# Optimization experiments

Measured on AMD Instinct MI355X. Metric: run time of the kernel, lower is better.

Reference implementation:

```python
import jax, jax.numpy as jnp
import numpy as np

B, D, N = 2, 512, 2048
H, MQ, MV = 8, 64, 64
SCALE = 1.0 / np.sqrt(D).astype(np.float32)  # 1/sqrt(num_dim_q), full dim


def setup_inputs() -> dict:
    key = jax.random.key(0)
    ks = jax.random.split(key, 9)
    s = 0.02
    return {
        "Q": jax.random.normal(ks[0], (B, D, N), jnp.float32),
        "Wq": jax.random.normal(ks[1], (MQ * H, D), jnp.float32) * s,
        "bq": jnp.zeros((MQ * H,), jnp.float32),
        "Wk": jax.random.normal(ks[2], (MQ * H, D), jnp.float32) * s,
        "bk": jnp.zeros((MQ * H,), jnp.float32),
        "Wv": jax.random.normal(ks[3], (MV * H, D), jnp.float32) * s,
        "bv": jnp.zeros((MV * H,), jnp.float32),
        "Wo": jax.random.normal(ks[4], (D, MV * H), jnp.float32) * s,
        "bo": jnp.zeros((D,), jnp.float32),
    }


def _conv1x1(x, W, b):
    # Conv1d with kernel_size=1 == per-position linear: [B,Cin,N] -> [B,Cout,N]
    return jnp.einsum("bcn,oc->bon", x, W) + b[None, :, None]


def reference(Q, Wq, bq, Wk, bk, Wv, bv, Wo, bo):
    q = _conv1x1(Q, Wq, bq)  # [B, MQ*H, N]
    k = _conv1x1(Q, Wk, bk)
    v = _conv1x1(Q, Wv, bv)  # [B, MV*H, N]
    b = Q.shape[0]
    n = Q.shape[2]
    # channel index factors as (dim, head): channel = d*H + h (matches torch .view)
    q = q.reshape(b, MQ, H, n)
    k = k.reshape(b, MQ, H, n)
    v = v.reshape(b, MV, H, n)
    scores = jnp.einsum("bdhq,bdhk->bhqk", q, k) * SCALE  # [B,H,Nq,Nk]
    attn = jax.nn.softmax(scores, axis=-1)
    o = jnp.einsum("bhqk,bdhk->bdhq", attn, v)  # [B, MV, H, Nq]
    o = o.reshape(b, MV * H, n)
    return _conv1x1(o, Wo, bo)  # [B, D, N]
```

## Files before the change

### kernel.cpp

```cpp
#include <hip/hip_runtime.h>

#define DEV __device__ __forceinline__

typedef __bf16 bf16;
typedef __bf16 bf16x8 __attribute__((ext_vector_type(8)));
typedef __bf16 bf16x4 __attribute__((ext_vector_type(4)));
typedef float f32x4 __attribute__((ext_vector_type(4)));
typedef float f32x16 __attribute__((ext_vector_type(16)));
typedef unsigned int u32x4 __attribute__((ext_vector_type(4)));

#define SCALE_F (0.04419417382415922f * 1.4426950408889634f)

DEV void gload_lds16(const void* g, void* l) {
  __builtin_amdgcn_global_load_lds(
      (const __attribute__((address_space(1))) void*)g,
      (__attribute__((address_space(3))) void*)l, 16, 0, 0);
}

DEV f32x4 mfma16(bf16x8 a, bf16x8 b, f32x4 c) {
  return __builtin_amdgcn_mfma_f32_16x16x32_bf16(a, b, c, 0, 0, 0);
}
DEV f32x16 mfma32(bf16x8 a, bf16x8 b, f32x16 c) {
  return __builtin_amdgcn_mfma_f32_32x32x16_bf16(a, b, c, 0, 0, 0);
}

DEV unsigned int pkbf(float a, float b) {
  unsigned short ua = __builtin_bit_cast(unsigned short, (bf16)a);
  unsigned short ub = __builtin_bit_cast(unsigned short, (bf16)b);
  return (unsigned int)ua | ((unsigned int)ub << 16);
}

__global__ __launch_bounds__(256) void prep(
    const float* __restrict__ Q,
    const float* __restrict__ Wq, const float* __restrict__ bq,
    const float* __restrict__ Wk, const float* __restrict__ bk,
    const float* __restrict__ Wv, const float* __restrict__ bv,
    const float* __restrict__ Wo,
    bf16* __restrict__ Wf, float* __restrict__ biasf, bf16* __restrict__ Wor,
    bf16* __restrict__ Qt) {
  __shared__ float tile[64][65];
  int bid = blockIdx.x;
  int t = threadIdx.x;
  if (bid < 256) {
    int r0 = bid * 8;
    for (int idx = t; idx < 1024; idx += 256) {
      int rl = idx >> 7, c4 = idx & 127;
      int row = r0 + rl;
      if (row < 1536) {
        const float* src;
        float scale = 1.0f;
        if (row < 512)       { src = Wq + (size_t)row * 512; scale = SCALE_F; }
        else if (row < 1024) { src = Wk + (size_t)(row - 512) * 512; }
        else                 { src = Wv + (size_t)(row - 1024) * 512; }
        float4 v = ((const float4*)src)[c4];
        bf16x4 o;
        o[0] = (bf16)(v.x * scale);
        o[1] = (bf16)(v.y * scale);
        o[2] = (bf16)(v.z * scale);
        o[3] = (bf16)(v.w * scale);
        *(bf16x4*)(Wf + (size_t)row * 512 + c4 * 4) = o;
      } else {
        int r = row - 1536;
#pragma unroll
        for (int e = 0; e < 4; ++e) {
          int c2 = c4 * 4 + e;
          Wor[(size_t)r * 512 + c2] =
              (bf16)Wo[(size_t)r * 512 + (c2 & 63) * 8 + (c2 >> 6)];
        }
      }
    }
    if (t < 8 && r0 + t < 1536) {
      int row = r0 + t;
      float bb;
      if (row < 512)       bb = bq[row] * SCALE_F;
      else if (row < 1024) bb = bk[row - 512];
      else                 bb = bv[row - 1024];
      biasf[row] = bb;
    }
  } else {
    int id2 = bid - 256;
    int n0 = (id2 & 31) * 64;
    int d0 = ((id2 >> 5) & 7) * 64;
    int b = id2 >> 8;
    int r = t >> 2, cw = t & 3;
    const float* src = Q + ((size_t)(b * 512 + d0 + r)) * 2048 + n0 + cw * 16;
#pragma unroll
    for (int e4 = 0; e4 < 4; ++e4) {
      float4 v = *(const float4*)(src + e4 * 4);
      tile[r][cw * 16 + e4 * 4 + 0] = v.x;
      tile[r][cw * 16 + e4 * 4 + 1] = v.y;
      tile[r][cw * 16 + e4 * 4 + 2] = v.z;
      tile[r][cw * 16 + e4 * 4 + 3] = v.w;
    }
    __syncthreads();
    bf16x8 o0{}, o1{};
#pragma unroll
    for (int e = 0; e < 8; ++e) {
      o0[e] = (bf16)tile[cw * 16 + e][r];
      o1[e] = (bf16)tile[cw * 16 + 8 + e][r];
    }
    bf16* dst = Qt + ((size_t)(b * 2048 + n0 + r)) * 512 + d0 + cw * 16;
    *(bf16x8*)dst = o0;
    *((bf16x8*)dst + 1) = o1;
  }
}

__global__ __launch_bounds__(256) void qkv_gemm(
    const bf16* __restrict__ Wf, const bf16* __restrict__ Qt,
    const float* __restrict__ biasf,
    bf16* __restrict__ qp, bf16* __restrict__ kp, bf16* __restrict__ vt) {
  __shared__ bf16 Al[128 * 64];
  __shared__ bf16 Bl[64 * 64];
  int hbid = blockIdx.x;
  int o = (hbid & 7) * 96 + (hbid >> 3);
  int cx = o % 12;
  int py = (o / 12) & 31;
  int b = o / 384;
  int c0 = cx * 128;
  int p0 = py * 64;
  int tid = threadIdx.x, w = tid >> 6, lane = tid & 63;
  int wm = w >> 1, wn = w & 1;
  int g = lane >> 4, l15 = lane & 15;

  const bf16* Abase = Wf + (size_t)c0 * 512;
  const bf16* Bbase = Qt + ((size_t)b * 2048 + p0) * 512;

  int srow = tid >> 3;
  int sch = tid & 7;

  f32x4 acc[4][2] = {};

  for (int ks = 0; ks < 8; ++ks) {
    int k0 = ks * 64;
    __syncthreads();
#pragma unroll
    for (int i = 0; i < 4; ++i) {
      int row = srow + i * 32;
      int ch = sch ^ (row & 7);
      gload_lds16(Abase + (size_t)row * 512 + k0 + ch * 8,
                  Al + (i * 32 + w * 8) * 64);
    }
#pragma unroll
    for (int i = 0; i < 2; ++i) {
      int row = srow + i * 32;
      int ch = sch ^ (row & 7);
      gload_lds16(Bbase + (size_t)row * 512 + k0 + ch * 8,
                  Bl + (i * 32 + w * 8) * 64);
    }
    __syncthreads();
#pragma unroll
    for (int ks2 = 0; ks2 < 2; ++ks2) {
      bf16x8 a[4], bb[2];
#pragma unroll
      for (int mi = 0; mi < 4; ++mi) {
        int row = wm * 64 + mi * 16 + l15;
        a[mi] = *(const bf16x8*)(Al + row * 64 +
                                 (((ks2 * 4 + g) ^ (row & 7)) << 3));
      }
#pragma unroll
      for (int ni = 0; ni < 2; ++ni) {
        int row = wn * 32 + ni * 16 + l15;
        bb[ni] = *(const bf16x8*)(Bl + row * 64 +
                                  (((ks2 * 4 + g) ^ (row & 7)) << 3));
      }
#pragma unroll
      for (int mi = 0; mi < 4; ++mi)
#pragma unroll
        for (int ni = 0; ni < 2; ++ni)
          acc[mi][ni] = mfma16(a[mi], bb[ni], acc[mi][ni]);
    }
  }

#pragma unroll
  for (int mi = 0; mi < 4; ++mi) {
#pragma unroll
    for (int ni = 0; ni < 2; ++ni) {
#pragma unroll
      for (int r = 0; r < 4; ++r) {
        int row = c0 + wm * 64 + mi * 16 + g * 4 + r;
        int p = p0 + wn * 32 + ni * 16 + l15;
        float val = acc[mi][ni][r] + biasf[row];
        bf16 hv = (bf16)val;
        if (row < 512) {
          int c = row;
          qp[(((size_t)b * 8 + (c & 7)) * 2048 + p) * 64 + (c >> 3)] = hv;
        } else if (row < 1024) {
          int c = row - 512;
          kp[(((size_t)b * 8 + (c & 7)) * 2048 + p) * 64 + (c >> 3)] = hv;
        } else {
          int c = row - 1024;
          int d = c >> 3, hh = c & 7;
          vt[((((size_t)b * 8 + hh) * 32 + (p >> 6)) * 64 + d) * 64 +
             (p & 63)] = hv;
        }
      }
    }
  }
}

__global__ __launch_bounds__(512, 4) void attn_k(
    const bf16* __restrict__ qp, const bf16* __restrict__ kp,
    const bf16* __restrict__ vt, bf16* __restrict__ Op,
    float* __restrict__ mbuf, float* __restrict__ lbuf, int TS) {
  __shared__ bf16 Ks[4][64 * 64];
  __shared__ bf16 Vs[4][64 * 64];
  int hbid = blockIdx.x;
  int o = (hbid & 7) * 64 + (hbid >> 3);
  int q0 = (o & 7) * 256;
  int bh = (o >> 3) & 15;
  int z = o >> 7;
  int tid = threadIdx.x, w = tid >> 6, lane = tid & 63;
  int l31 = lane & 31, hi = lane >> 5;

  bf16x8 qreg[4];
#pragma unroll
  for (int kd = 0; kd < 4; ++kd)
    qreg[kd] = *(const bf16x8*)(
        qp + ((size_t)bh * 2048 + q0 + w * 32 + l31) * 64 + kd * 16 + hi * 8);

  int krow = tid >> 3;
  int kch = (tid & 7) ^ (krow & 7);

  const bf16* Kall = kp + (size_t)bh * 2048 * 64 + (size_t)z * TS * 4096;
  const bf16* Vall = vt + ((size_t)bh * 32 + (size_t)z * TS) * 4096;

  gload_lds16(Kall + (size_t)krow * 64 + kch * 8, Ks[0] + w * 512);
  gload_lds16(Vall + (size_t)krow * 64 + kch * 8, Vs[0] + w * 512);
  gload_lds16(Kall + 4096 + (size_t)krow * 64 + kch * 8, Ks[1] + w * 512);
  gload_lds16(Vall + 4096 + (size_t)krow * 64 + kch * 8, Vs[1] + w * 512);

  f32x16 oacc0 = {}, oacc1 = {};
  float mrow = -1e30f, rs = 0.0f;

  for (int t = 0; t < TS; ++t) {
    int cur = t & 3;
    int nb = (t + 2) & 3;
    int tp = (t + 2 < TS) ? t + 2 : TS - 1;

    gload_lds16(Kall + (size_t)tp * 4096 + (size_t)krow * 64 + kch * 8,
                Ks[nb] + w * 512);
    gload_lds16(Vall + (size_t)tp * 4096 + (size_t)krow * 64 + kch * 8,
                Vs[nb] + w * 512);

    asm volatile("s_waitcnt vmcnt(4)" ::: "memory");
    __builtin_amdgcn_s_barrier();
    __builtin_amdgcn_sched_barrier(0);
    asm volatile("" ::: "memory");

    f32x16 st0 = {}, st1 = {};
    __builtin_amdgcn_s_setprio(1);
#pragma unroll
    for (int kd = 0; kd < 4; ++kd) {
      int sw = ((kd * 2 + hi) ^ (l31 & 7)) << 3;
      bf16x8 kb0 = *(const bf16x8*)(Ks[cur] + l31 * 64 + sw);
      bf16x8 kb1 = *(const bf16x8*)(Ks[cur] + (32 + l31) * 64 + sw);
      st0 = mfma32(kb0, qreg[kd], st0);
      st1 = mfma32(kb1, qreg[kd], st1);
    }
    __builtin_amdgcn_s_setprio(0);

    float rm = st0[0];
#pragma unroll
    for (int r = 1; r < 16; ++r) rm = fmaxf(rm, st0[r]);
#pragma unroll
    for (int r = 0; r < 16; ++r) rm = fmaxf(rm, st1[r]);
    rm = fmaxf(rm, __shfl_xor(rm, 32));

    if (__any(rm > mrow + 8.0f)) {
      float nm = fmaxf(mrow, rm);
      float esc = __builtin_amdgcn_exp2f(mrow - nm);
      mrow = nm;
      rs *= esc;
#pragma unroll
      for (int r = 0; r < 16; ++r) {
        int ql = (r & 3) + 8 * (r >> 2) + 4 * hi;
        float er = __shfl(esc, ql, 64);
        oacc0[r] *= er;
        oacc1[r] *= er;
      }
    }

    bf16x8 pa[4];
#pragma unroll
    for (int tile = 0; tile < 2; ++tile) {
      float pv[16];
#pragma unroll
      for (int r = 0; r < 16; ++r) {
        float v = __builtin_amdgcn_exp2f((tile ? st1[r] : st0[r]) - mrow);
        pv[r] = v;
        rs += v;
      }
      unsigned int r0d0 = pkbf(pv[0], pv[1]),   r0d1 = pkbf(pv[2], pv[3]);
      unsigned int r1d0 = pkbf(pv[4], pv[5]),   r1d1 = pkbf(pv[6], pv[7]);
      unsigned int r2d0 = pkbf(pv[8], pv[9]),   r2d1 = pkbf(pv[10], pv[11]);
      unsigned int r3d0 = pkbf(pv[12], pv[13]), r3d1 = pkbf(pv[14], pv[15]);
      asm volatile("v_permlane32_swap_b32 %0, %1" : "+v"(r0d0), "+v"(r1d0));
      asm volatile("v_permlane32_swap_b32 %0, %1" : "+v"(r0d1), "+v"(r1d1));
      pa[tile * 2] = __builtin_bit_cast(bf16x8, (u32x4){r0d0, r0d1, r1d0, r1d1});
      asm volatile("v_permlane32_swap_b32 %0, %1" : "+v"(r2d0), "+v"(r3d0));
      asm volatile("v_permlane32_swap_b32 %0, %1" : "+v"(r2d1), "+v"(r3d1));
      pa[tile * 2 + 1] =
          __builtin_bit_cast(bf16x8, (u32x4){r2d0, r2d1, r3d0, r3d1});
    }

    __builtin_amdgcn_s_setprio(1);
#pragma unroll
    for (int kt = 0; kt < 4; ++kt) {
      int sw0 = ((kt * 2 + hi) ^ (l31 & 7)) << 3;
      bf16x8 vb0 = *(const bf16x8*)(Vs[cur] + l31 * 64 + sw0);
      bf16x8 vb1 = *(const bf16x8*)(Vs[cur] + (32 + l31) * 64 + sw0);
      oacc0 = mfma32(pa[kt], vb0, oacc0);
      oacc1 = mfma32(pa[kt], vb1, oacc1);
    }
    __builtin_amdgcn_s_setprio(0);
    asm volatile("" ::: "memory");
  }

  rs += __shfl_xor(rs, 32);

  size_t zb = (size_t)(z * 16 + bh) * 2048 + q0 + w * 32;
#pragma unroll
  for (int r = 0; r < 16; ++r) {
    int ql = (r & 3) + 8 * (r >> 2) + 4 * hi;
    Op[(zb + ql) * 64 + l31] = (bf16)oacc0[r];
    Op[(zb + ql) * 64 + 32 + l31] = (bf16)oacc1[r];
  }
  if (hi == 0) {
    mbuf[zb + l31] = mrow;
    lbuf[zb + l31] = rs;
  }
}

__global__ __launch_bounds__(256) void combine(
    const bf16* __restrict__ Op, const float* __restrict__ mbuf,
    const float* __restrict__ lbuf, bf16* __restrict__ oh, int NS) {
  int idx = blockIdx.x * 256 + threadIdx.x;
  int row = idx >> 2;
  int dc = (idx & 3) * 16;

  float M = -1e30f;
  for (int z = 0; z < NS; ++z) M = fmaxf(M, mbuf[(size_t)z * 32768 + row]);

  float L = 0.0f;
  float acc[16];
#pragma unroll
  for (int e = 0; e < 16; ++e) acc[e] = 0.0f;

  for (int z = 0; z < NS; ++z) {
    float wz = __builtin_amdgcn_exp2f(mbuf[(size_t)z * 32768 + row] - M);
    L += wz * lbuf[(size_t)z * 32768 + row];
    const bf16x8* p = (const bf16x8*)(Op + ((size_t)z * 32768 + row) * 64 + dc);
#pragma unroll
    for (int v = 0; v < 2; ++v) {
      bf16x8 x = p[v];
#pragma unroll
      for (int e = 0; e < 8; ++e) acc[v * 8 + e] += wz * (float)x[e];
    }
  }
  float invL = 1.0f / L;
  bf16x8* po = (bf16x8*)(oh + (size_t)row * 64 + dc);
#pragma unroll
  for (int v = 0; v < 2; ++v) {
    bf16x8 o;
#pragma unroll
    for (int e = 0; e < 8; ++e) o[e] = (bf16)(acc[v * 8 + e] * invL);
    po[v] = o;
  }
}

__global__ __launch_bounds__(256) void out_gemm(
    const bf16* __restrict__ Wor, const bf16* __restrict__ oh,
    const float* __restrict__ bo, float* __restrict__ out) {
  __shared__ bf16 Al[128 * 64];
  __shared__ bf16 Bl[64 * 64];
  int hbid = blockIdx.x;
  int o = (hbid & 7) * 32 + (hbid >> 3);
  int r0 = (o & 3) * 128;
  int p0 = ((o >> 2) & 31) * 64;
  int b = o >> 7;
  int tid = threadIdx.x, w = tid >> 6, lane = tid & 63;
  int wm = w >> 1, wn = w & 1;
  int g = lane >> 4, l15 = lane & 15;

  const bf16* Abase = Wor + (size_t)r0 * 512;

  int srow = tid >> 3;
  int sch = tid & 7;

  f32x4 acc[4][2] = {};

  for (int ks = 0; ks < 8; ++ks) {
    int k0 = ks * 64;
    const bf16* Bbase = oh + (((size_t)b * 8 + ks) * 2048 + p0) * 64;
    __syncthreads();
#pragma unroll
    for (int i = 0; i < 4; ++i) {
      int row = srow + i * 32;
      int ch = sch ^ (row & 7);
      gload_lds16(Abase + (size_t)row * 512 + k0 + ch * 8,
                  Al + (i * 32 + w * 8) * 64);
    }
#pragma unroll
    for (int i = 0; i < 2; ++i) {
      int row = srow + i * 32;
      int ch = sch ^ (row & 7);
      gload_lds16(Bbase + (size_t)row * 64 + ch * 8,
                  Bl + (i * 32 + w * 8) * 64);
    }
    __syncthreads();
#pragma unroll
    for (int ks2 = 0; ks2 < 2; ++ks2) {
      bf16x8 a[4], bb[2];
#pragma unroll
      for (int mi = 0; mi < 4; ++mi) {
        int row = wm * 64 + mi * 16 + l15;
        a[mi] = *(const bf16x8*)(Al + row * 64 +
                                 (((ks2 * 4 + g) ^ (row & 7)) << 3));
      }
#pragma unroll
      for (int ni = 0; ni < 2; ++ni) {
        int row = wn * 32 + ni * 16 + l15;
        bb[ni] = *(const bf16x8*)(Bl + row * 64 +
                                  (((ks2 * 4 + g) ^ (row & 7)) << 3));
      }
#pragma unroll
      for (int mi = 0; mi < 4; ++mi)
#pragma unroll
        for (int ni = 0; ni < 2; ++ni)
          acc[mi][ni] = mfma16(a[mi], bb[ni], acc[mi][ni]);
    }
  }

#pragma unroll
  for (int mi = 0; mi < 4; ++mi) {
#pragma unroll
    for (int ni = 0; ni < 2; ++ni) {
#pragma unroll
      for (int r = 0; r < 4; ++r) {
        int row = r0 + wm * 64 + mi * 16 + g * 4 + r;
        int p = p0 + wn * 32 + ni * 16 + l15;
        out[((size_t)b * 512 + row) * 2048 + p] = acc[mi][ni][r] + bo[row];
      }
    }
  }
}

extern "C" void kernel_launch(void* const* d_in, const int* in_sizes, int n_in,
                              void* d_out, int out_size, void* d_ws, size_t ws_size,
                              hipStream_t stream) {
  (void)in_sizes; (void)n_in; (void)out_size;
  const float* Q  = (const float*)d_in[0];
  const float* Wq = (const float*)d_in[1];
  const float* bq = (const float*)d_in[2];
  const float* Wk = (const float*)d_in[3];
  const float* bk = (const float*)d_in[4];
  const float* Wv = (const float*)d_in[5];
  const float* bv = (const float*)d_in[6];
  const float* Wo = (const float*)d_in[7];
  const float* bo = (const float*)d_in[8];
  float* out = (float*)d_out;

  char* ws = (char*)d_ws;
  bf16*  Wf    = (bf16*)(ws + 0);
  bf16*  Wor   = (bf16*)(ws + 1572864);
  float* biasf = (float*)(ws + 2097152);
  bf16*  Qt    = (bf16*)(ws + 2103296);
  bf16*  qp    = (bf16*)(ws + 6297600);
  bf16*  kp    = (bf16*)(ws + 10491904);
  bf16*  vt    = (bf16*)(ws + 14686208);

  size_t need4 = 18880512ull + 4ull * 4194304 + 2ull * 4ull * 131072;
  int NS = (ws_size >= need4) ? 4 : 2;
  int TS = 32 / NS;

  bf16*  Opart = (bf16*)(ws + 18880512);
  float* mbuf  = (float*)(ws + 18880512 + (size_t)NS * 4194304);
  float* lbuf  = (float*)(ws + 18880512 + (size_t)NS * 4194304 +
                          (size_t)NS * 131072);
  bf16*  oh    = Opart;

  prep<<<dim3(768), dim3(256), 0, stream>>>(Q, Wq, bq, Wk, bk, Wv, bv, Wo,
                                            Wf, biasf, Wor, Qt);
  qkv_gemm<<<dim3(768), dim3(256), 0, stream>>>(Wf, Qt, biasf, qp, kp, vt);
  attn_k<<<dim3(16 * NS * 8), dim3(512), 0, stream>>>(qp, kp, vt, Opart, mbuf,
                                                      lbuf, TS);
  combine<<<dim3(512), dim3(256), 0, stream>>>(Opart, mbuf, lbuf, oh, NS);
  out_gemm<<<dim3(256), dim3(256), 0, stream>>>(Wor, oh, bo, out);
}
```

Baseline: 71.01 us.

## Software-pipeline QKV and output GEMMs with 4-stage LDS ring buffer

Both projection GEMMs move from a single-buffered 64-wide K loop with two barriers per step to a 32-wide K step over a 4-slot LDS ring. Loads run two stages ahead, and each step uses a partial vmcnt wait plus a single barrier. This lets global-to-LDS copies overlap the MFMA work. The swizzle is adapted to 32-element rows, and the last iterations reload stage 15 redundantly, so correctness depends on the hand-placed waitcnt and barrier ordering.

```diff
diff --git a/kernel.cpp b/kernel.cpp
--- a/kernel.cpp
+++ b/kernel.cpp
@@ -109,8 +109,8 @@
     const bf16* __restrict__ Wf, const bf16* __restrict__ Qt,
     const float* __restrict__ biasf,
     bf16* __restrict__ qp, bf16* __restrict__ kp, bf16* __restrict__ vt) {
-  __shared__ bf16 Al[128 * 64];
-  __shared__ bf16 Bl[64 * 64];
+  __shared__ bf16 Al[4][128 * 32];
+  __shared__ bf16 Bl[4][64 * 32];
   int hbid = blockIdx.x;
   int o = (hbid & 7) * 96 + (hbid >> 3);
   int cx = o % 12;
@@ -125,50 +125,70 @@
   const bf16* Abase = Wf + (size_t)c0 * 512;
   const bf16* Bbase = Qt + ((size_t)b * 2048 + p0) * 512;
 
-  int srow = tid >> 3;
-  int sch = tid & 7;
+  int srow = tid >> 2;
+  int sc = tid & 3;
 
   f32x4 acc[4][2] = {};
 
-  for (int ks = 0; ks < 8; ++ks) {
-    int k0 = ks * 64;
-    __syncthreads();
-#pragma unroll
-    for (int i = 0; i < 4; ++i) {
-      int row = srow + i * 32;
-      int ch = sch ^ (row & 7);
+#pragma unroll
+  for (int t0 = 0; t0 < 2; ++t0) {
+    int k0 = t0 * 32;
+#pragma unroll
+    for (int i = 0; i < 2; ++i) {
+      int row = i * 64 + srow;
+      int ch = sc ^ ((row >> 1) & 3);
       gload_lds16(Abase + (size_t)row * 512 + k0 + ch * 8,
-                  Al + (i * 32 + w * 8) * 64);
-    }
+                  Al[t0] + (i * 64 + w * 16) * 32);
+    }
+    {
+      int ch = sc ^ ((srow >> 1) & 3);
+      gload_lds16(Bbase + (size_t)srow * 512 + k0 + ch * 8,
+                  Bl[t0] + w * 16 * 32);
+    }
+  }
+
+  for (int ks = 0; ks < 16; ++ks) {
+    int cur = ks & 3;
+    int nb = (ks + 2) & 3;
+    int kp2 = (ks + 2 < 16) ? ks + 2 : 15;
+    int k0n = kp2 * 32;
 #pragma unroll
     for (int i = 0; i < 2; ++i) {
-      int row = srow + i * 32;
-      int ch = sch ^ (row & 7);
-      gload_lds16(Bbase + (size_t)row * 512 + k0 + ch * 8,
-                  Bl + (i * 32 + w * 8) * 64);
-    }
-    __syncthreads();
-#pragma unroll
-    for (int ks2 = 0; ks2 < 2; ++ks2) {
-      bf16x8 a[4], bb[2];
-#pragma unroll
-      for (int mi = 0; mi < 4; ++mi) {
-        int row = wm * 64 + mi * 16 + l15;
-        a[mi] = *(const bf16x8*)(Al + row * 64 +
-                                 (((ks2 * 4 + g) ^ (row & 7)) << 3));
-      }
-#pragma unroll
-      for (int ni = 0; ni < 2; ++ni) {
-        int row = wn * 32 + ni * 16 + l15;
-        bb[ni] = *(const bf16x8*)(Bl + row * 64 +
-                                  (((ks2 * 4 + g) ^ (row & 7)) << 3));
-      }
-#pragma unroll
-      for (int mi = 0; mi < 4; ++mi)
-#pragma unroll
-        for (int ni = 0; ni < 2; ++ni)
-          acc[mi][ni] = mfma16(a[mi], bb[ni], acc[mi][ni]);
-    }
+      int row = i * 64 + srow;
+      int ch = sc ^ ((row >> 1) & 3);
+      gload_lds16(Abase + (size_t)row * 512 + k0n + ch * 8,
+                  Al[nb] + (i * 64 + w * 16) * 32);
+    }
+    {
+      int ch = sc ^ ((srow >> 1) & 3);
+      gload_lds16(Bbase + (size_t)srow * 512 + k0n + ch * 8,
+                  Bl[nb] + w * 16 * 32);
+    }
+
+    asm volatile("s_waitcnt vmcnt(6)" ::: "memory");
+    __builtin_amdgcn_s_barrier();
+    __builtin_amdgcn_sched_barrier(0);
+    asm volatile("" ::: "memory");
+
+    bf16x8 a[4], bb[2];
+#pragma unroll
+    for (int mi = 0; mi < 4; ++mi) {
+      int row = wm * 64 + mi * 16 + l15;
+      a[mi] = *(const bf16x8*)(Al[cur] + row * 32 +
+                               ((g ^ ((row >> 1) & 3)) << 3));
+    }
+#pragma unroll
+    for (int ni = 0; ni < 2; ++ni) {
+      int row = wn * 32 + ni * 16 + l15;
+      bb[ni] = *(const bf16x8*)(Bl[cur] + row * 32 +
+                                ((g ^ ((row >> 1) & 3)) << 3));
+    }
+#pragma unroll
+    for (int mi = 0; mi < 4; ++mi)
+#pragma unroll
+      for (int ni = 0; ni < 2; ++ni)
+        acc[mi][ni] = mfma16(a[mi], bb[ni], acc[mi][ni]);
+    asm volatile("" ::: "memory");
   }
 
 #pragma unroll
@@ -371,8 +391,8 @@
 __global__ __launch_bounds__(256) void out_gemm(
     const bf16* __restrict__ Wor, const bf16* __restrict__ oh,
     const float* __restrict__ bo, float* __restrict__ out) {
-  __shared__ bf16 Al[128 * 64];
-  __shared__ bf16 Bl[64 * 64];
+  __shared__ bf16 Al[4][128 * 32];
+  __shared__ bf16 Bl[4][64 * 32];
   int hbid = blockIdx.x;
   int o = (hbid & 7) * 32 + (hbid >> 3);
   int r0 = (o & 3) * 128;
@@ -383,52 +403,74 @@
   int g = lane >> 4, l15 = lane & 15;
 
   const bf16* Abase = Wor + (size_t)r0 * 512;
-
-  int srow = tid >> 3;
-  int sch = tid & 7;
+  const bf16* Bhead = oh + ((size_t)b * 8 * 2048 + p0) * 64;
+
+  int srow = tid >> 2;
+  int sc = tid & 3;
 
   f32x4 acc[4][2] = {};
 
-  for (int ks = 0; ks < 8; ++ks) {
-    int k0 = ks * 64;
-    const bf16* Bbase = oh + (((size_t)b * 8 + ks) * 2048 + p0) * 64;
-    __syncthreads();
-#pragma unroll
-    for (int i = 0; i < 4; ++i) {
-      int row = srow + i * 32;
-      int ch = sch ^ (row & 7);
+#pragma unroll
+  for (int t0 = 0; t0 < 2; ++t0) {
+    int k0 = t0 * 32;
+    int hh = k0 >> 6, d0 = k0 & 63;
+#pragma unroll
+    for (int i = 0; i < 2; ++i) {
+      int row = i * 64 + srow;
+      int ch = sc ^ ((row >> 1) & 3);
       gload_lds16(Abase + (size_t)row * 512 + k0 + ch * 8,
-                  Al + (i * 32 + w * 8) * 64);
-    }
+                  Al[t0] + (i * 64 + w * 16) * 32);
+    }
+    {
+      int ch = sc ^ ((srow >> 1) & 3);
+      gload_lds16(Bhead + ((size_t)hh * 2048 + srow) * 64 + d0 + ch * 8,
+                  Bl[t0] + w * 16 * 32);
+    }
+  }
+
+  for (int ks = 0; ks < 16; ++ks) {
+    int cur = ks & 3;
+    int nb = (ks + 2) & 3;
+    int kq = (ks + 2 < 16) ? ks + 2 : 15;
+    int k0n = kq * 32;
+    int hhn = k0n >> 6, d0n = k0n & 63;
 #pragma unroll
     for (int i = 0; i < 2; ++i) {
-      int row = srow + i * 32;
-      int ch = sch ^ (row & 7);
-      gload_lds16(Bbase + (size_t)row * 64 + ch * 8,
-                  Bl + (i * 32 + w * 8) * 64);
-    }
-    __syncthreads();
-#pragma unroll
-    for (int ks2 = 0; ks2 < 2; ++ks2) {
-      bf16x8 a[4], bb[2];
-#pragma unroll
-      for (int mi = 0; mi < 4; ++mi) {
-        int row = wm * 64 + mi * 16 + l15;
-        a[mi] = *(const bf16x8*)(Al + row * 64 +
-                                 (((ks2 * 4 + g) ^ (row & 7)) << 3));
-      }
-#pragma unroll
-      for (int ni = 0; ni < 2; ++ni) {
-        int row = wn * 32 + ni * 16 + l15;
-        bb[ni] = *(const bf16x8*)(Bl + row * 64 +
-                                  (((ks2 * 4 + g) ^ (row & 7)) << 3));
-      }
-#pragma unroll
-      for (int mi = 0; mi < 4; ++mi)
-#pragma unroll
-        for (int ni = 0; ni < 2; ++ni)
-          acc[mi][ni] = mfma16(a[mi], bb[ni], acc[mi][ni]);
-    }
+      int row = i * 64 + srow;
+      int ch = sc ^ ((row >> 1) & 3);
+      gload_lds16(Abase + (size_t)row * 512 + k0n + ch * 8,
+                  Al[nb] + (i * 64 + w * 16) * 32);
+    }
+    {
+      int ch = sc ^ ((srow >> 1) & 3);
+      gload_lds16(Bhead + ((size_t)hhn * 2048 + srow) * 64 + d0n + ch * 8,
+                  Bl[nb] + w * 16 * 32);
+    }
+
+    asm volatile("s_waitcnt vmcnt(6)" ::: "memory");
+    __builtin_amdgcn_s_barrier();
+    __builtin_amdgcn_sched_barrier(0);
+    asm volatile("" ::: "memory");
+
+    bf16x8 a[4], bb[2];
+#pragma unroll
+    for (int mi = 0; mi < 4; ++mi) {
+      int row = wm * 64 + mi * 16 + l15;
+      a[mi] = *(const bf16x8*)(Al[cur] + row * 32 +
+                               ((g ^ ((row >> 1) & 3)) << 3));
+    }
+#pragma unroll
+    for (int ni = 0; ni < 2; ++ni) {
+      int row = wn * 32 + ni * 16 + l15;
+      bb[ni] = *(const bf16x8*)(Bl[cur] + row * 32 +
+                                ((g ^ ((row >> 1) & 3)) << 3));
+    }
+#pragma unroll
+    for (int mi = 0; mi < 4; ++mi)
+#pragma unroll
+      for (int ni = 0; ni < 2; ++ni)
+        acc[mi][ni] = mfma16(a[mi], bb[ni], acc[mi][ni]);
+    asm volatile("" ::: "memory");
   }
 
 #pragma unroll
```

Result: slower. 74.56 us (+5.0%).
